# Performance work log

Measured on AMD Instinct MI355X. Metric: run time of the kernel, lower is better.

The kernel has to match this reference:

```python
import jax, jax.numpy as jnp
import numpy as np
from jax import lax

B, T, E, H, V = 1024, 128, 300, 100, 50000
K = 4  # topk in catch()
NEG_INF = -1e30


def setup_inputs() -> dict:
    key = jax.random.key(0)
    ks = jax.random.split(key, 12)
    word_id = jax.random.randint(ks[0], (B, T), 0, V, dtype=jnp.int32)
    sen_len = jax.random.randint(ks[1], (B,), K, T + 1, dtype=jnp.int32)  # >= K for topk
    label_word_id = jax.random.randint(ks[2], (B, 1), 0, V, dtype=jnp.int32)
    emb = jax.random.normal(ks[3], (V, E), jnp.float32) * 0.1
    W_ih = jax.random.normal(ks[4], (4 * H, E), jnp.float32) * 0.05
    W_hh = jax.random.normal(ks[5], (4 * H, H), jnp.float32) * 0.05
    b_ih = jax.random.normal(ks[6], (4 * H,), jnp.float32) * 0.05
    b_hh = jax.random.normal(ks[7], (4 * H,), jnp.float32) * 0.05
    lin_W = jax.random.normal(ks[8], (6, H), jnp.float32) * 0.1
    lin_b = jax.random.normal(ks[9], (6,), jnp.float32) * 0.1
    ll_W = jax.random.normal(ks[10], (H, E), jnp.float32) * 0.05
    ll_b = jax.random.normal(ks[11], (H,), jnp.float32) * 0.05
    return dict(word_id=word_id, sen_len=sen_len, label_word_id=label_word_id,
                emb=emb, W_ih=W_ih, W_hh=W_hh, b_ih=b_ih, b_hh=b_hh,
                lin_W=lin_W, lin_b=lin_b, ll_W=ll_W, ll_b=ll_b)


def _lstm(x, W_ih, W_hh, b_ih, b_hh):
    # x: (B, T, E) -> out: (B, T, H). Single layer, pytorch gate order i,f,g,o.
    b = b_ih + b_hh
    def step(carry, x_t):
        h, c = carry
        gates = x_t @ W_ih.T + h @ W_hh.T + b  # (B, 4H)
        i, f, g, o = jnp.split(gates, 4, axis=-1)
        c = jax.nn.sigmoid(f) * c + jax.nn.sigmoid(i) * jnp.tanh(g)
        h = jax.nn.sigmoid(o) * jnp.tanh(c)
        return (h, c), h
    h0 = jnp.zeros((x.shape[0], W_hh.shape[1]), x.dtype)
    (_, _), hs = lax.scan(step, (h0, h0), x.transpose(1, 0, 2))
    return hs.transpose(1, 0, 2)


def reference(word_id, sen_len, label_word_id, emb, W_ih, W_hh, b_ih, b_hh,
              lin_W, lin_b, ll_W, ll_b):
    word_vec = emb[word_id]                      # (B, T, E)
    out = _lstm(word_vec, W_ih, W_hh, b_ih, b_hh)  # (B, T, H)

    # last valid hidden state -> linear
    last = out[jnp.arange(out.shape[0]), sen_len - 1]  # (B, H)
    out_f = last @ lin_W.T + lin_b               # (B, 6)

    # label vector through llinear
    label_vec = emb[label_word_id[:, 0]] @ ll_W.T + ll_b  # (B, H)

    # --- catch(), vectorized ---
    scores = jnp.einsum('bth,bh->bt', out, label_vec)     # (B, T)
    valid = jnp.arange(out.shape[1])[None, :] < sen_len[:, None]  # (B, T)
    vals, idx = lax.top_k(jnp.where(valid, scores, NEG_INF), K)   # (B, K)
    s_value = jnp.take_along_axis(out, idx[:, :, None], axis=1)   # (B, K, H)
    pos = jnp.sum(s_value * vals[:, :, None], axis=1)             # (B, H)

    # neg: valid positions excluding topk; original bug: vector_list accumulates
    # across the batch loop -> cumulative sum over batch dimension.
    top_mask = jnp.zeros(valid.shape, bool).at[
        jnp.arange(valid.shape[0])[:, None], idx].set(True)
    neg_mask = valid & ~top_mask                                   # (B, T)
    per_neg = jnp.einsum('bth,bt->bh', out, neg_mask.astype(out.dtype))
    neg = jnp.cumsum(per_neg, axis=0)                              # (B, H)

    l_rep = pos @ lin_W.T + lin_b
    r_rep = neg @ lin_W.T + lin_b
    return (out_f, l_rep, r_rep)
```

## Files before the change

### kernel.cpp

```cpp
#include <hip/hip_runtime.h>
#include <hip/hip_bf16.h>
#include <cstdint>

#define Bn   1024
#define Tn   128
#define En   300
#define Hn   100
#define Vn   50000
#define G4n  400
#define MPn  50048
#define NPn  448

typedef __bf16 bf16x8 __attribute__((ext_vector_type(8)));
typedef _Float16 half8 __attribute__((ext_vector_type(8)));
typedef _Float16 half2v __attribute__((ext_vector_type(2)));
typedef float  f32x4  __attribute__((ext_vector_type(4)));

#define OFF_TABLE  0ull
#define OFF_OH16   44800000ull
#define OFF_WFRAG  71014400ull
#define OFF_WFRAGB 71129088ull
#define OFF_LLWT   71415808ull
#define OFF_LV     71535808ull
#define OFF_PN     71945408ull
#define OFF_NEG    72355008ull

__device__ __forceinline__ float sigf(float x) { return 1.0f / (1.0f + __expf(-x)); }
__device__ __forceinline__ float tanhfast(float x) { return 1.0f - 2.0f / (__expf(2.0f * x) + 1.0f); }

#define BAR_LDS() do {                                         \
    asm volatile("s_waitcnt lgkmcnt(0)" ::: "memory");          \
    __builtin_amdgcn_s_barrier();                               \
    asm volatile("" ::: "memory");                              \
} while (0)

__global__ void k_prep(const float* __restrict__ W_ih, const float* __restrict__ W_hh,
                       const float* __restrict__ llW,
                       uint4* __restrict__ wfrag, uint4* __restrict__ wfragB,
                       float* __restrict__ llwt) {
    int idx = blockIdx.x * 256 + threadIdx.x;
    if (idx < 28 * 4 * 64) {
        int lane = idx & 63, tk = idx >> 6;
        int nt = tk >> 2, kc = tk & 3;
        int n = nt * 16 + (lane & 15);
        int k0 = kc * 32 + (lane >> 4) * 8;
        int q = n & 3, u = n >> 2;
        union { _Float16 h[8]; uint4 v; } pk;
#pragma unroll
        for (int j = 0; j < 8; j++) {
            int k = k0 + j;
            pk.h[j] = (_Float16)((u < Hn && k < Hn) ? W_hh[(size_t)(q * Hn + u) * Hn + k] : 0.0f);
        }
        wfrag[idx] = pk.v;
    }
    if (idx < 10 * 28 * 64) {
        int lane = idx & 63, tk = idx >> 6;
        int kc = tk / 28, nsg = tk - kc * 28;
        int n = nsg * 16 + (lane & 15);
        int k0 = kc * 32 + (lane >> 4) * 8;
        int q = n & 3, u = n >> 2;
        union { __bf16 h[8]; uint4 v; } pk;
#pragma unroll
        for (int j = 0; j < 8; j++) {
            int k = k0 + j;
            pk.h[j] = (__bf16)((u < Hn && k < En) ? W_ih[(size_t)(q * Hn + u) * En + k] : 0.0f);
        }
        wfragB[idx] = pk.v;
    }
    if (idx < En * Hn) {
        int k = idx / Hn, h = idx - k * Hn;
        llwt[idx] = llW[(size_t)h * En + k];
    }
}

__global__ __launch_bounds__(256, 2) void k_table(
    const float* __restrict__ emb, const uint4* __restrict__ wfragB,
    const float* __restrict__ b_ih, const float* __restrict__ b_hh,
    _Float16* __restrict__ table) {
    __shared__ __bf16 a_sh[64][328];
    const int tid = threadIdx.x;
    const int mt = blockIdx.x >> 1, nh = blockIdx.x & 1;

#pragma unroll
    for (int it = 0; it < 5; it++) {
        int x = it * 256 + tid;
        int row = x / 20, seg = x - row * 20;
        int gr = mt * 64 + row;
        const float* ar = emb + (size_t)(gr < Vn ? gr : Vn - 1) * En;
        int c0 = seg * 16;
        union { __bf16 h[16]; bf16x8 v[2]; } pk;
#pragma unroll
        for (int g = 0; g < 4; g++) {
            int c = c0 + g * 4;
            if (c + 4 <= En) {
                float4 f = *(const float4*)(ar + c);
                pk.h[g * 4 + 0] = (__bf16)f.x; pk.h[g * 4 + 1] = (__bf16)f.y;
                pk.h[g * 4 + 2] = (__bf16)f.z; pk.h[g * 4 + 3] = (__bf16)f.w;
            } else {
                pk.h[g * 4 + 0] = (__bf16)0.f; pk.h[g * 4 + 1] = (__bf16)0.f;
                pk.h[g * 4 + 2] = (__bf16)0.f; pk.h[g * 4 + 3] = (__bf16)0.f;
            }
        }
        *(bf16x8*)&a_sh[row][c0] = pk.v[0];
        *(bf16x8*)&a_sh[row][c0 + 8] = pk.v[1];
    }
    __syncthreads();

    const int wv = tid >> 6, l = tid & 63;
    const int c16 = l & 15, quad = l >> 4;
    f32x4 acc[14];
#pragma unroll
    for (int i = 0; i < 14; i++) acc[i] = (f32x4){0.f, 0.f, 0.f, 0.f};

    uint4 bcur[14];
#pragma unroll
    for (int ns = 0; ns < 14; ns++) bcur[ns] = wfragB[((0 * 28 + nh * 14 + ns) << 6) + l];

    for (int kc = 0; kc < 10; kc++) {
        uint4 bnxt[14];
        if (kc < 9) {
#pragma unroll
            for (int ns = 0; ns < 14; ns++) bnxt[ns] = wfragB[(((kc + 1) * 28 + nh * 14 + ns) << 6) + l];
        }
        bf16x8 af = *(const bf16x8*)&a_sh[wv * 16 + c16][kc * 32 + quad * 8];
#pragma unroll
        for (int ns = 0; ns < 14; ns++)
            acc[ns] = __builtin_amdgcn_mfma_f32_16x16x32_bf16(af, __builtin_bit_cast(bf16x8, bcur[ns]), acc[ns], 0, 0, 0);
        if (kc < 9) {
#pragma unroll
            for (int ns = 0; ns < 14; ns++) bcur[ns] = bnxt[ns];
        }
    }
#pragma unroll
    for (int ns = 0; ns < 14; ns++) {
        int n = (nh * 14 + ns) * 16 + c16;
        int q = n & 3, u = n >> 2;
        if (u < Hn) {
            int j = q * Hn + u;
            float bias = b_ih[j] + b_hh[j];
#pragma unroll
            for (int r = 0; r < 4; r++) {
                int m = mt * 64 + wv * 16 + quad * 4 + r;
                if (m < Vn) table[(size_t)m * NPn + n] = (_Float16)(acc[ns][r] + bias);
            }
        }
    }
}

__global__ void k_label(const int* __restrict__ lwid, const float* __restrict__ emb,
                        const float* __restrict__ llwt, const float* __restrict__ llb,
                        float* __restrict__ lv) {
    __shared__ float er[En];
    __shared__ float part[Hn];
    int b = blockIdx.x;
    int lid = lwid[b];
    for (int k = threadIdx.x; k < En; k += 256) er[k] = emb[(size_t)lid * En + k];
    __syncthreads();
    int h = threadIdx.x & 127, half = threadIdx.x >> 7;
    float acc = 0.f;
    if (h < Hn) {
        int k0 = half * 150, k1 = k0 + 150;
        for (int k = k0; k < k1; k++) acc += er[k] * llwt[k * Hn + h];
        if (half == 1) part[h] = acc;
    }
    __syncthreads();
    if (h < Hn && half == 0) lv[(size_t)b * Hn + h] = acc + part[h] + llb[h];
}

__global__ __launch_bounds__(256, 2) void k_lstm(
    const int* __restrict__ word_id, const int* __restrict__ sen_len,
    const _Float16* __restrict__ table, const uint4* __restrict__ wfrag,
    const float* __restrict__ lv, const float* __restrict__ linW,
    const float* __restrict__ linb, _Float16* __restrict__ oh16,
    float* __restrict__ per_neg, float* __restrict__ d_out) {
    __shared__ float    gbufs[4][280];
    __shared__ _Float16 h_cur[2][2][136];
    __shared__ float    lt_sh[2][Hn];
    __shared__ float    spw[2][Tn][4];
    __shared__ int      widc[2][Tn];
    __shared__ float    pos_sh[2][Hn];
    __shared__ float    lasth_sh[2][Hn];
    __shared__ float    tk_val[2][4];
    __shared__ int      tk_idx[2][4];

    const int tid = threadIdx.x;
    const int w = tid >> 6, l = tid & 63;
    const int c16 = l & 15, quad = l >> 4;
    const int b0 = blockIdx.x * 2;

    for (int i = tid; i < 272; i += 256) ((uint32_t*)h_cur)[i] = 0u;
    if (tid < 200) {
        int imb = (tid >= Hn), iu = tid - imb * Hn;
        lt_sh[imb][iu] = lv[(size_t)(b0 + imb) * Hn + iu];
    }
    { int imb = tid >> 7, it = tid & 127; widc[imb][it] = word_id[(b0 + imb) * Tn + it]; }

    half8 bfr[7][4];
#pragma unroll
    for (int n7 = 0; n7 < 7; n7++)
#pragma unroll
        for (int kc = 0; kc < 4; kc++)
            bfr[n7][kc] = __builtin_bit_cast(half8, wfrag[((w * 7 + n7) * 4 + kc) * 64 + l]);

    const int u_loc = l >> 1, mb = l & 1;
    const int u = w * 28 + u_loc;
    const bool act = (l < 56) && (u < Hn);
    const int myslen = act ? sen_len[b0 + mb] : 0;
    float* gb = &gbufs[w][0];

    __syncthreads();

    uint2 xq = {0, 0};
    if (act) xq = *(const uint2*)(table + (size_t)widc[mb][0] * NPn + u * 4);

    float c_reg = 0.f, sumh = 0.f, lasth = 0.f;
    _Float16* ohb_w = oh16 + (size_t)(b0 + mb) * Tn * Hn;

    for (int t = 0; t < Tn; t++) {
        const _Float16* hp = &h_cur[t & 1][0][0];
        f32x4 acc[7];
#pragma unroll
        for (int n7 = 0; n7 < 7; n7++) acc[n7] = (f32x4){0.f, 0.f, 0.f, 0.f};
#pragma unroll
        for (int kc = 0; kc < 4; kc++) {
            half8 af = *(const half8*)(hp + (c16 & 1) * 136 + kc * 32 + quad * 8);
#pragma unroll
            for (int n7 = 0; n7 < 7; n7++)
                acc[n7] = __builtin_amdgcn_mfma_f32_16x16x32_f16(af, bfr[n7][kc], acc[n7], 0, 0, 0);
        }
        if (l < 16) {
#pragma unroll
            for (int n7 = 0; n7 < 7; n7++) {
                int nl = n7 * 16 + l;
                int adr = (nl >> 2) * 5 + (nl & 3);
                gb[adr] = acc[n7][0];
                gb[140 + adr] = acc[n7][1];
            }
        }
        float p = 0.f;
        if (act) {
            int base = mb * 140 + u_loc * 5;
            half2v x01 = __builtin_bit_cast(half2v, xq.x);
            half2v x23 = __builtin_bit_cast(half2v, xq.y);
            float gi = gb[base] + (float)x01.x;
            float gf = gb[base + 1] + (float)x01.y;
            float gg = gb[base + 2] + (float)x23.x;
            float go = gb[base + 3] + (float)x23.y;
            float c = sigf(gf) * c_reg + sigf(gi) * tanhfast(gg);
            c_reg = c;
            float hh = sigf(go) * tanhfast(c);
            h_cur[(t + 1) & 1][mb][u] = (_Float16)hh;
            ohb_w[t * Hn + u] = (_Float16)hh;
            if (t < myslen) sumh += hh;
            if (t == myslen - 1) lasth = hh;
            p = hh * lt_sh[mb][u];
            int tn = (t + 1 < Tn) ? t + 1 : t;
            xq = *(const uint2*)(table + (size_t)widc[mb][tn] * NPn + u * 4);
        }
        p += __shfl_down(p, 32, 64);
        p += __shfl_down(p, 16, 64);
        p += __shfl_down(p, 8, 64);
        p += __shfl_down(p, 4, 64);
        p += __shfl_down(p, 2, 64);
        if (l < 2) spw[l][t][w] = p;
        BAR_LDS();
    }
    if (w < 2) {
        int kmb = w, lane = l;
        int sl = sen_len[b0 + kmb];
        float4 p0 = *(const float4*)&spw[kmb][lane][0];
        float4 p1 = *(const float4*)&spw[kmb][lane + 64][0];
        float s0 = (lane < sl) ? (p0.x + p0.y + p0.z + p0.w) : -1e30f;
        float s1 = (lane + 64 < sl) ? (p1.x + p1.y + p1.z + p1.w) : -1e30f;
        bool tk0 = false, tk1 = false;
#pragma unroll
        for (int p4 = 0; p4 < 4; p4++) {
            float v = tk0 ? -1e30f : s0;
            int ix = lane;
            float v1 = tk1 ? -1e30f : s1;
            if (v1 > v) { v = v1; ix = lane + 64; }
            for (int off = 32; off; off >>= 1) {
                float ov = __shfl_down(v, off, 64);
                int oi = __shfl_down(ix, off, 64);
                if (ov > v || (ov == v && oi < ix)) { v = ov; ix = oi; }
            }
            v = __shfl(v, 0, 64);
            ix = __shfl(ix, 0, 64);
            if (lane == 0) { tk_val[kmb][p4] = v; tk_idx[kmb][p4] = ix; }
            if (ix == lane) tk0 = true;
            if (ix == lane + 64) tk1 = true;
        }
    }
    __syncthreads();
    if (act) {
        float pos = 0.f, nsum = sumh;
#pragma unroll
        for (int p4 = 0; p4 < 4; p4++) {
            int ix = tk_idx[mb][p4];
            float r = (float)ohb_w[ix * Hn + u];
            pos += tk_val[mb][p4] * r;
            nsum -= r;
        }
        pos_sh[mb][u] = pos;
        lasth_sh[mb][u] = lasth;
        per_neg[(size_t)(b0 + mb) * Hn + u] = nsum;
    }
    __syncthreads();
    if (tid < 24) {
        int which = tid / 12, r = tid - which * 12;
        int pmb = r / 6, o = r - pmb * 6;
        const float* src = which ? &pos_sh[pmb][0] : &lasth_sh[pmb][0];
        float acc2 = linb[o];
        for (int uu = 0; uu < Hn; uu++) acc2 += src[uu] * linW[o * Hn + uu];
        d_out[(which ? (Bn * 6) : 0) + (b0 + pmb) * 6 + o] = acc2;
    }
}

__global__ __launch_bounds__(1024) void k_scan(const float* __restrict__ pn, float* __restrict__ neg) {
    __shared__ float wsum[16];
    __shared__ float wpre[16];
    int u = blockIdx.x, t = threadIdx.x;
    int lane = t & 63, wv = t >> 6;
    float v = pn[(size_t)t * Hn + u];
#pragma unroll
    for (int off = 1; off < 64; off <<= 1) {
        float o = __shfl_up(v, off, 64);
        if (lane >= off) v += o;
    }
    if (lane == 63) wsum[wv] = v;
    __syncthreads();
    if (t < 16) {
        float s = wsum[t];
#pragma unroll
        for (int off = 1; off < 16; off <<= 1) {
            float o = __shfl_up(s, off, 64);
            if (t >= off) s += o;
        }
        wpre[t] = s;
    }
    __syncthreads();
    float pre = wv ? wpre[wv - 1] : 0.f;
    neg[(size_t)t * Hn + u] = v + pre;
}

__global__ void k_rrep(const float* __restrict__ neg, const float* __restrict__ linW,
                       const float* __restrict__ linb, float* __restrict__ d_out) {
    int gid = blockIdx.x * 256 + threadIdx.x;
    if (gid < Bn * 6) {
        int b = gid / 6, o = gid - b * 6;
        float acc = linb[o];
        for (int u = 0; u < Hn; u++) acc += neg[(size_t)b * Hn + u] * linW[o * Hn + u];
        d_out[2 * Bn * 6 + gid] = acc;
    }
}

extern "C" void kernel_launch(void* const* d_in, const int* in_sizes, int n_in,
                              void* d_out, int out_size, void* d_ws, size_t ws_size,
                              hipStream_t stream) {
    const int*   word_id = (const int*)d_in[0];
    const int*   sen_len = (const int*)d_in[1];
    const int*   lwid    = (const int*)d_in[2];
    const float* emb     = (const float*)d_in[3];
    const float* W_ih    = (const float*)d_in[4];
    const float* W_hh    = (const float*)d_in[5];
    const float* b_ih    = (const float*)d_in[6];
    const float* b_hh    = (const float*)d_in[7];
    const float* linW    = (const float*)d_in[8];
    const float* linb    = (const float*)d_in[9];
    const float* llW     = (const float*)d_in[10];
    const float* llb     = (const float*)d_in[11];

    char* ws = (char*)d_ws;
    _Float16* table  = (_Float16*)(ws + OFF_TABLE);
    _Float16* oh16   = (_Float16*)(ws + OFF_OH16);
    uint4*    wfrag  = (uint4*)(ws + OFF_WFRAG);
    uint4*    wfragB = (uint4*)(ws + OFF_WFRAGB);
    float*    llwt   = (float*)(ws + OFF_LLWT);
    float*    lvp    = (float*)(ws + OFF_LV);
    float*    pn     = (float*)(ws + OFF_PN);
    float*    neg    = (float*)(ws + OFF_NEG);
    float*    outp   = (float*)d_out;

    k_prep<<<118, 256, 0, stream>>>(W_ih, W_hh, llW, wfrag, wfragB, llwt);
    k_table<<<(MPn / 64) * 2, 256, 0, stream>>>(emb, wfragB, b_ih, b_hh, table);
    k_label<<<Bn, 256, 0, stream>>>(lwid, emb, llwt, llb, lvp);
    k_lstm<<<Bn / 2, 256, 0, stream>>>(word_id, sen_len, table, wfrag, lvp, linW, linb, oh16, pn, outp);
    k_scan<<<Hn, 1024, 0, stream>>>(pn, neg);
    k_rrep<<<(Bn * 6 + 255) / 256, 256, 0, stream>>>(neg, linW, linb, outp);
}
```

Measured before the change: 308.9 us.

## Defer score reduction via DPP off the critical path, prefetch embeddings two steps ahead

The per-step attention score reduction no longer uses a chain of cross-lane shuffles right after the gate update. Instead the previous step's partial product is reduced inside 16-lane rows with DPP row-shift adds, placed right after the MFMA issue, and written as 16 partials per timestep that the top-k stage later sums. The label vector value now lives in a register instead of LDS, and the embedding gather is double-buffered two steps ahead. The aim is to shorten the serial per-timestep critical path of the recurrence. The cost is more LDS for the partials, an extra reduction in the epilogue, and more registers live across the loop.

```diff
diff --git a/kernel.cpp b/kernel.cpp
--- a/kernel.cpp
+++ b/kernel.cpp
@@ -32,6 +32,12 @@
     asm volatile("s_waitcnt lgkmcnt(0)" ::: "memory");          \
     __builtin_amdgcn_s_barrier();                               \
     asm volatile("" ::: "memory");                              \
+} while (0)
+
+#define DPP_ADD_SHL(v, N) do {                                                     \
+    int _s = __builtin_amdgcn_update_dpp(0, __builtin_bit_cast(int, (v)),          \
+                                         0x100 | (N), 0xF, 0xF, true);             \
+    (v) += __builtin_bit_cast(float, _s);                                          \
 } while (0)
 
 __global__ void k_prep(const float* __restrict__ W_ih, const float* __restrict__ W_hh,
@@ -175,8 +181,7 @@
     float* __restrict__ per_neg, float* __restrict__ d_out) {
     __shared__ float    gbufs[4][280];
     __shared__ _Float16 h_cur[2][2][136];
-    __shared__ float    lt_sh[2][Hn];
-    __shared__ float    spw[2][Tn][4];
+    __shared__ float    spw[2][Tn][16];
     __shared__ int      widc[2][Tn];
     __shared__ float    pos_sh[2][Hn];
     __shared__ float    lasth_sh[2][Hn];
@@ -189,10 +194,6 @@
     const int b0 = blockIdx.x * 2;
 
     for (int i = tid; i < 272; i += 256) ((uint32_t*)h_cur)[i] = 0u;
-    if (tid < 200) {
-        int imb = (tid >= Hn), iu = tid - imb * Hn;
-        lt_sh[imb][iu] = lv[(size_t)(b0 + imb) * Hn + iu];
-    }
     { int imb = tid >> 7, it = tid & 127; widc[imb][it] = word_id[(b0 + imb) * Tn + it]; }
 
     half8 bfr[7][4];
@@ -206,14 +207,19 @@
     const int u = w * 28 + u_loc;
     const bool act = (l < 56) && (u < Hn);
     const int myslen = act ? sen_len[b0 + mb] : 0;
+    const float lt_reg = act ? lv[(size_t)(b0 + mb) * Hn + u] : 0.f;
     float* gb = &gbufs[w][0];
 
     __syncthreads();
 
-    uint2 xq = {0, 0};
-    if (act) xq = *(const uint2*)(table + (size_t)widc[mb][0] * NPn + u * 4);
+    uint2 xq = {0, 0}, xq1 = {0, 0};
+    if (act) {
+        xq  = *(const uint2*)(table + (size_t)widc[mb][0] * NPn + u * 4);
+        xq1 = *(const uint2*)(table + (size_t)widc[mb][1] * NPn + u * 4);
+    }
 
     float c_reg = 0.f, sumh = 0.f, lasth = 0.f;
+    float p_carry = 0.f;
     _Float16* ohb_w = oh16 + (size_t)(b0 + mb) * Tn * Hn;
 
     for (int t = 0; t < Tn; t++) {
@@ -227,6 +233,13 @@
 #pragma unroll
             for (int n7 = 0; n7 < 7; n7++)
                 acc[n7] = __builtin_amdgcn_mfma_f32_16x16x32_f16(af, bfr[n7][kc], acc[n7], 0, 0, 0);
+        }
+        {
+            float pr = p_carry;
+            DPP_ADD_SHL(pr, 2);
+            DPP_ADD_SHL(pr, 4);
+            DPP_ADD_SHL(pr, 8);
+            if ((l & 15) < 2 && t > 0) spw[l & 1][t - 1][w * 4 + quad] = pr;
         }
         if (l < 16) {
 #pragma unroll
@@ -253,25 +266,37 @@
             ohb_w[t * Hn + u] = (_Float16)hh;
             if (t < myslen) sumh += hh;
             if (t == myslen - 1) lasth = hh;
-            p = hh * lt_sh[mb][u];
-            int tn = (t + 1 < Tn) ? t + 1 : t;
-            xq = *(const uint2*)(table + (size_t)widc[mb][tn] * NPn + u * 4);
-        }
-        p += __shfl_down(p, 32, 64);
-        p += __shfl_down(p, 16, 64);
-        p += __shfl_down(p, 8, 64);
-        p += __shfl_down(p, 4, 64);
-        p += __shfl_down(p, 2, 64);
-        if (l < 2) spw[l][t][w] = p;
+            p = hh * lt_reg;
+            int tn2 = (t + 2 < Tn) ? t + 2 : Tn - 1;
+            xq = xq1;
+            xq1 = *(const uint2*)(table + (size_t)widc[mb][tn2] * NPn + u * 4);
+        }
+        p_carry = p;
         BAR_LDS();
     }
+    {
+        float pr = p_carry;
+        DPP_ADD_SHL(pr, 2);
+        DPP_ADD_SHL(pr, 4);
+        DPP_ADD_SHL(pr, 8);
+        if ((l & 15) < 2) spw[l & 1][Tn - 1][w * 4 + quad] = pr;
+    }
+    __syncthreads();
     if (w < 2) {
         int kmb = w, lane = l;
         int sl = sen_len[b0 + kmb];
-        float4 p0 = *(const float4*)&spw[kmb][lane][0];
-        float4 p1 = *(const float4*)&spw[kmb][lane + 64][0];
-        float s0 = (lane < sl) ? (p0.x + p0.y + p0.z + p0.w) : -1e30f;
-        float s1 = (lane + 64 < sl) ? (p1.x + p1.y + p1.z + p1.w) : -1e30f;
+        const float* s16a = &spw[kmb][lane][0];
+        const float* s16b = &spw[kmb][lane + 64][0];
+        float4 a0 = *(const float4*)(s16a + 0), a1 = *(const float4*)(s16a + 4);
+        float4 a2 = *(const float4*)(s16a + 8), a3 = *(const float4*)(s16a + 12);
+        float4 b0v = *(const float4*)(s16b + 0), b1v = *(const float4*)(s16b + 4);
+        float4 b2v = *(const float4*)(s16b + 8), b3v = *(const float4*)(s16b + 12);
+        float sa = (a0.x + a0.y + a0.z + a0.w) + (a1.x + a1.y + a1.z + a1.w)
+                 + (a2.x + a2.y + a2.z + a2.w) + (a3.x + a3.y + a3.z + a3.w);
+        float sb = (b0v.x + b0v.y + b0v.z + b0v.w) + (b1v.x + b1v.y + b1v.z + b1v.w)
+                 + (b2v.x + b2v.y + b2v.z + b2v.w) + (b3v.x + b3v.y + b3v.z + b3v.w);
+        float s0 = (lane < sl) ? sa : -1e30f;
+        float s1 = (lane + 64 < sl) ? sb : -1e30f;
         bool tk0 = false, tk1 = false;
 #pragma unroll
         for (int p4 = 0; p4 < 4; p4++) {
```

Result: no change. 309.1 us (+0.1%).
